# Optimization experiments

Measured on AMD Instinct MI355X. Metric: run time of the kernel, lower is better.

Reference implementation:

```python
import jax, jax.numpy as jnp
import numpy as np

NUM_HEADS = 12   # H
NUM_TASKS = 4    # T
TOP_K = 2        # capacity_factor


def setup_inputs() -> dict:
    key = jax.random.key(0)
    ks = jax.random.split(key, 4)
    B, N, C = 2, 4100, 768  # N = NUM_TASKS + M, M = 4096
    x = jax.random.normal(ks[0], (B, N, C), dtype=jnp.float32)
    # torch.nn.Linear weights are [out_features, in_features]; y = x @ W.T
    qs_w = jax.random.normal(ks[1], (NUM_TASKS, C, C), dtype=jnp.float32) * 0.02
    kv_w = jax.random.normal(ks[2], (2 * C, C), dtype=jnp.float32) * 0.02
    experts_w = jax.random.normal(ks[3], (NUM_TASKS, C, C), dtype=jnp.float32) * 0.02
    return {"x": x, "qs_w": qs_w, "kv_w": kv_w, "experts_w": experts_w}


def reference(x, qs_w, kv_w, experts_w):
    B, N, C = x.shape
    T, H, K = NUM_TASKS, NUM_HEADS, TOP_K
    d = C // H
    M = N - T
    scale = d ** -0.5

    feature = x[:, T:, :]                                    # [B,M,C]
    kv = (feature @ kv_w.T).reshape(B, M, 2, H, d)
    k = jnp.transpose(kv[:, :, 0], (0, 2, 1, 3))             # [B,H,M,d]
    v = jnp.transpose(kv[:, :, 1], (0, 2, 1, 3))             # [B,H,M,d]

    # per-task q projections on task tokens (qs_w[t] is [out,in])
    q = jnp.einsum('btc,toc->bto', x[:, :T], qs_w)           # [B,T,C]
    q = q.reshape(B, T, H, d).transpose(0, 2, 1, 3)          # [B,H,T,d]

    attn = jnp.einsum('bhtd,bhmd->bhtm', q, k) * scale       # [B,H,T,M]
    topv, topi = jax.lax.top_k(attn, K)                      # [B,H,T,K]
    topw = jax.nn.softmax(topv, axis=-1)                     # softmax over top-k only

    # scatter softmaxed top-k back into dense [B,H,T,M] (indices unique per row)
    oh = jax.nn.one_hot(topi, M, dtype=x.dtype)              # [B,H,T,K,M]
    attn_topk = jnp.einsum('bhtk,bhtkm->bhtm', topw, oh)
    attn_token = jnp.einsum('bhtm,bhmd->bhtd', attn_topk, v)
    attn_token = attn_token.transpose(0, 2, 1, 3).reshape(B, T, C)   # [B,T,C]

    # gather top-k feature rows per head/task, weight, and scatter back
    fm = feature.reshape(B, M, H, d).transpose(0, 2, 1, 3)   # [B,H,M,d]
    feat_topk = jnp.take_along_axis(fm[:, :, None], topi[..., None], axis=3)  # [B,H,T,K,d]
    feat_topk = feat_topk * topw[..., None]
    # scatter to [B,H,T,M,d], then permute(0,2,3,1,4)+reshape -> [B,T,M,C]
    feat_pad = jnp.einsum('bhtkd,bhtkm->btmhd', feat_topk, oh).reshape(B, T, M, C)

    # per-task experts (no bias); einsum('btnc,btnc->bnc') with ones = sum over t
    feature_output = jnp.einsum('btmc,toc->bmo', feat_pad, experts_w)  # [B,M,C]
    token_output = jnp.einsum('btc,toc->bto', attn_token, experts_w)   # [B,T,C]

    return jnp.concatenate([token_output, feature_output], axis=1)     # [B,N,C]
```

## Files before the change

### kernel.cpp

```cpp
#include <hip/hip_runtime.h>
#include <math.h>

#define B_ 2
#define N_ 4100
#define C_ 768
#define T_ 4
#define H_ 12
#define D_ 64
#define M_ 4096
#define S_ 48
#define KS_ 6
#define KC_ 128
#define SCALE 0.125f

__device__ __forceinline__ bool better(float va, int ia, float vb, int ib) {
  return (va > vb) || (va == vb && ia < ib);
}

__device__ __forceinline__ void merge2(float& v1, int& i1, float& v2, int& i2,
                                       float ov1, int oi1, float ov2, int oi2) {
  if (better(ov1, oi1, v1, i1)) {
    float tv; int ti;
    tv = v1; ti = i1; v1 = ov1; i1 = oi1; ov1 = tv; oi1 = ti;
    tv = v2; ti = i2; v2 = ov2; i2 = oi2; ov2 = tv; oi2 = ti;
  }
  if (better(ov1, oi1, v2, i2)) { v2 = ov1; i2 = oi1; }
}

__global__ __launch_bounds__(256) void q_kernel(const float* __restrict__ x,
    const float* __restrict__ qs_w, float* __restrict__ qbuf) {
  const int oc = blockIdx.x % 12;
  const int t = (blockIdx.x / 12) % T_;
  const int b = blockIdx.x / (12 * T_);
  const int tid = threadIdx.x;
  __shared__ float xs[C_];
  __shared__ float red[256];
  for (int i = tid; i < C_; i += 256) xs[i] = x[((size_t)b * N_ + t) * C_ + i];
  __syncthreads();
  const int j = tid & 63;
  const int pt = tid >> 6;
  const int o = oc * 64 + j;
  const float* wr = qs_w + ((size_t)t * C_ + o) * C_ + pt * 192;
  float a = 0.f;
  for (int c = 0; c < 192; ++c) a += xs[pt * 192 + c] * wr[c];
  red[tid] = a;
  __syncthreads();
  if (tid < 64) {
    float v = (red[tid] + red[tid + 64] + red[tid + 128] + red[tid + 192]) * SCALE;
    qbuf[((size_t)b * T_ + t) * C_ + o] = v;
  }
}

__global__ __launch_bounds__(256) void qk_kernel(const float* __restrict__ qbuf,
    const float* __restrict__ kv_w, float* __restrict__ qk) {
  const int h = blockIdx.x % H_;
  const int t = (blockIdx.x / H_) % T_;
  const int b = blockIdx.x / (T_ * H_);
  const int tid = threadIdx.x;
  __shared__ float qs[D_];
  if (tid < 64) qs[tid] = qbuf[((size_t)b * T_ + t) * C_ + h * 64 + tid];
  __syncthreads();
  for (int c = tid; c < C_; c += 256) {
    float a = 0.f;
    #pragma unroll 8
    for (int j = 0; j < 64; ++j) a += qs[j] * kv_w[((size_t)(h * 64 + j)) * C_ + c];
    qk[(((size_t)b * T_ + t) * H_ + h) * C_ + c] = a;
  }
}

__global__ __launch_bounds__(256) void score_kernel(const float* __restrict__ x,
    const float* __restrict__ qk, float* __restrict__ part) {
  const int mt = blockIdx.x & 63;
  const int b = blockIdx.x >> 6;
  const int kc = blockIdx.y;
  const int tid = threadIdx.x;
  const int m0 = mt * 64;

  __shared__ __align__(16) float fbuf[64][68];
  __shared__ __align__(16) float qkbuf[48][68];

  const int mg = tid & 15;
  const int sg = tid >> 4;

  float acc[4][3];
  #pragma unroll
  for (int u = 0; u < 4; ++u)
    #pragma unroll
    for (int i = 0; i < 3; ++i) acc[u][i] = 0.f;

  const float* xb = x + ((size_t)b * N_ + T_ + m0) * C_ + kc * KC_;
  const float* qkb = qk + (size_t)b * S_ * C_ + kc * KC_;

  for (int cc = 0; cc < KC_ / 64; ++cc) {
    __syncthreads();
    for (int i = tid; i < 64 * 16; i += 256) {
      int row = i >> 4, c4 = i & 15;
      *(float4*)&fbuf[row][c4 * 4] =
          *(const float4*)(xb + (size_t)row * C_ + cc * 64 + c4 * 4);
    }
    for (int i = tid; i < 48 * 16; i += 256) {
      int s = i >> 4, c4 = i & 15;
      *(float4*)&qkbuf[s][c4 * 4] =
          *(const float4*)(qkb + (size_t)s * C_ + cc * 64 + c4 * 4);
    }
    __syncthreads();
    #pragma unroll 4
    for (int c4 = 0; c4 < 16; ++c4) {
      float4 f[4], q[3];
      f[0] = *(const float4*)&fbuf[mg][c4 * 4];
      f[1] = *(const float4*)&fbuf[mg + 16][c4 * 4];
      f[2] = *(const float4*)&fbuf[mg + 32][c4 * 4];
      f[3] = *(const float4*)&fbuf[mg + 48][c4 * 4];
      q[0] = *(const float4*)&qkbuf[sg * 3 + 0][c4 * 4];
      q[1] = *(const float4*)&qkbuf[sg * 3 + 1][c4 * 4];
      q[2] = *(const float4*)&qkbuf[sg * 3 + 2][c4 * 4];
      #pragma unroll
      for (int u = 0; u < 4; ++u)
        #pragma unroll
        for (int i = 0; i < 3; ++i)
          acc[u][i] += f[u].x * q[i].x + f[u].y * q[i].y +
                       f[u].z * q[i].z + f[u].w * q[i].w;
    }
  }

  #pragma unroll
  for (int i = 0; i < 3; ++i) {
    int s = sg * 3 + i;
    float* pp = part + (((size_t)kc * B_ + b) * S_ + s) * M_ + m0 + mg;
    #pragma unroll
    for (int u = 0; u < 4; ++u) pp[16 * u] = acc[u][i];
  }
}

__global__ __launch_bounds__(256) void top2_kernel(const float* __restrict__ part,
                                                   float* __restrict__ top2) {
  const int s = blockIdx.x % S_;
  const int b = blockIdx.x / S_;
  const int tid = threadIdx.x;
  float v1 = -INFINITY, v2 = -INFINITY;
  int i1 = 0x7fffffff, i2 = 0x7fffffff;
  const float* p0 = part + ((size_t)b * S_ + s) * M_;
  const size_t kstride = (size_t)B_ * S_ * M_;
  for (int m = tid; m < M_; m += 256) {
    float v = 0.f;
    #pragma unroll
    for (int kc = 0; kc < KS_; ++kc) v += p0[kc * kstride + m];
    if (better(v, m, v1, i1)) { v2 = v1; i2 = i1; v1 = v; i1 = m; }
    else if (better(v, m, v2, i2)) { v2 = v; i2 = m; }
  }
  #pragma unroll
  for (int off = 1; off < 64; off <<= 1) {
    float ov1 = __shfl_xor(v1, off);
    int   oi1 = __shfl_xor(i1, off);
    float ov2 = __shfl_xor(v2, off);
    int   oi2 = __shfl_xor(i2, off);
    merge2(v1, i1, v2, i2, ov1, oi1, ov2, oi2);
  }
  __shared__ float cbuf[4][4];
  const int w = tid >> 6, lane = tid & 63;
  if (lane == 0) {
    cbuf[w][0] = v1; ((int*)cbuf[w])[1] = i1;
    cbuf[w][2] = v2; ((int*)cbuf[w])[3] = i2;
  }
  __syncthreads();
  if (tid == 0) {
    for (int ww = 1; ww < 4; ++ww)
      merge2(v1, i1, v2, i2, cbuf[ww][0], ((int*)cbuf[ww])[1],
             cbuf[ww][2], ((int*)cbuf[ww])[3]);
    float w1 = 1.f / (1.f + expf(v2 - v1));
    float* tp = top2 + ((size_t)b * S_ + s) * 4;
    ((int*)tp)[0] = i1; ((int*)tp)[1] = i2;
    tp[2] = w1; tp[3] = 1.f - w1;
  }
}

__global__ __launch_bounds__(256) void gather_kernel(const float* __restrict__ x,
    const float* __restrict__ kv_w, const float* __restrict__ experts_w,
    const float* __restrict__ top2, float* __restrict__ attn, float* __restrict__ out) {
  const int h = blockIdx.x % H_;
  const int t = (blockIdx.x / H_) % T_;
  const int b = blockIdx.x / S_;
  const int tid = threadIdx.x;
  const float* tp = top2 + (size_t)blockIdx.x * 4;
  const int i1 = ((const int*)tp)[0];
  const int i2 = ((const int*)tp)[1];
  const float w1 = tp[2], w2 = tp[3];
  __shared__ float f0[C_], f1[C_], fc[C_], red[256];
  const float* r0 = x + ((size_t)b * N_ + T_ + i1) * C_;
  const float* r1 = x + ((size_t)b * N_ + T_ + i2) * C_;
  for (int i = tid; i < C_; i += 256) {
    float a = r0[i], bb = r1[i];
    f0[i] = a; f1[i] = bb; fc[i] = w1 * a + w2 * bb;
  }
  __syncthreads();
  const int j = tid & 63, pt = tid >> 6;
  {
    const float* kr = kv_w + ((size_t)(C_ + h * 64 + j)) * C_ + pt * 192;
    float a = 0.f;
    for (int c = 0; c < 192; ++c) a += fc[pt * 192 + c] * kr[c];
    red[tid] = a;
  }
  __syncthreads();
  if (tid < 64)
    attn[((size_t)b * T_ + t) * C_ + h * 64 + tid] =
        red[tid] + red[tid + 64] + red[tid + 128] + red[tid + 192];
  const size_t o0 = ((size_t)b * N_ + T_ + i1) * C_;
  const size_t o1 = ((size_t)b * N_ + T_ + i2) * C_;
  for (int o = tid; o < C_; o += 256) {
    const float* er = experts_w + ((size_t)t * C_ + o) * C_ + h * 64;
    float a0 = 0.f, a1 = 0.f;
    #pragma unroll 8
    for (int c = 0; c < 64; ++c) {
      float e = er[c];
      a0 += e * f0[h * 64 + c];
      a1 += e * f1[h * 64 + c];
    }
    atomicAdd(&out[o0 + o], w1 * a0);
    atomicAdd(&out[o1 + o], w2 * a1);
  }
}

__global__ __launch_bounds__(256) void token_kernel(const float* __restrict__ attn,
    const float* __restrict__ experts_w, float* __restrict__ out) {
  const int oc = blockIdx.x % 12;
  const int t = (blockIdx.x / 12) % T_;
  const int b = blockIdx.x / (12 * T_);
  const int tid = threadIdx.x;
  __shared__ float ar[C_];
  __shared__ float red[256];
  for (int i = tid; i < C_; i += 256) ar[i] = attn[((size_t)b * T_ + t) * C_ + i];
  __syncthreads();
  const int j = tid & 63, pt = tid >> 6;
  const int o = oc * 64 + j;
  const float* er = experts_w + ((size_t)t * C_ + o) * C_ + pt * 192;
  float a = 0.f;
  for (int c = 0; c < 192; ++c) a += ar[pt * 192 + c] * er[c];
  red[tid] = a;
  __syncthreads();
  if (tid < 64)
    out[((size_t)b * N_ + t) * C_ + oc * 64 + tid] =
        red[tid] + red[tid + 64] + red[tid + 128] + red[tid + 192];
}

extern "C" void kernel_launch(void* const* d_in, const int* in_sizes, int n_in,
                              void* d_out, int out_size, void* d_ws, size_t ws_size,
                              hipStream_t stream) {
  const float* x         = (const float*)d_in[0];
  const float* qs_w      = (const float*)d_in[1];
  const float* kv_w      = (const float*)d_in[2];
  const float* experts_w = (const float*)d_in[3];
  float* out = (float*)d_out;

  float* ws   = (float*)d_ws;
  float* qbuf = ws;
  float* qk   = qbuf + (size_t)B_ * T_ * C_;
  float* part = qk + (size_t)B_ * S_ * C_;
  float* top2 = part + (size_t)KS_ * B_ * S_ * M_;
  float* attn = top2 + (size_t)B_ * S_ * 4;

  hipMemsetAsync(d_out, 0, (size_t)out_size * sizeof(float), stream);

  hipLaunchKernelGGL(q_kernel,     dim3(B_ * T_ * 12),      dim3(256), 0, stream, x, qs_w, qbuf);
  hipLaunchKernelGGL(qk_kernel,    dim3(B_ * T_ * H_),      dim3(256), 0, stream, qbuf, kv_w, qk);
  hipLaunchKernelGGL(score_kernel, dim3(B_ * 64, KS_),      dim3(256), 0, stream, x, qk, part);
  hipLaunchKernelGGL(top2_kernel,  dim3(B_ * S_),           dim3(256), 0, stream, part, top2);
  hipLaunchKernelGGL(gather_kernel,dim3(B_ * S_),           dim3(256), 0, stream, x, kv_w, experts_w, top2, attn, out);
  hipLaunchKernelGGL(token_kernel, dim3(B_ * T_ * 12),      dim3(256), 0, stream, attn, experts_w, out);
}
```

Measured before the change: 166.4 us.

## Fuse q/qk, top2/gather/token kernels and split score reduction finer

Merges q projection into the qk kernel, with each block recomputing only its head's 64-wide q slice. Folds the top-2 selection and the token expert projection into the gather kernel, which now writes token outputs via atomics. Doubles the score kernel's K-split (KS 12, KC 64) so each block loads one tile, giving more blocks but more partial sums to reduce. Launches drop from six to three, at the cost of more partial-buffer traffic and extra atomics on the token rows.

```diff
diff --git a/kernel.cpp b/kernel.cpp
--- a/kernel.cpp
+++ b/kernel.cpp
@@ -9,8 +9,8 @@
 #define D_ 64
 #define M_ 4096
 #define S_ 48
-#define KS_ 6
-#define KC_ 128
+#define KS_ 12
+#define KC_ 64
 #define SCALE 0.125f
 
 __device__ __forceinline__ bool better(float va, int ia, float vb, int ib) {
@@ -27,44 +27,35 @@
   if (better(ov1, oi1, v2, i2)) { v2 = ov1; i2 = oi1; }
 }
 
-__global__ __launch_bounds__(256) void q_kernel(const float* __restrict__ x,
-    const float* __restrict__ qs_w, float* __restrict__ qbuf) {
-  const int oc = blockIdx.x % 12;
-  const int t = (blockIdx.x / 12) % T_;
-  const int b = blockIdx.x / (12 * T_);
+__global__ __launch_bounds__(256) void qk_kernel(const float* __restrict__ x,
+    const float* __restrict__ qs_w, const float* __restrict__ kv_w,
+    float* __restrict__ qk) {
+  const int h = blockIdx.x % H_;
+  const int t = (blockIdx.x / H_) % T_;
+  const int b = blockIdx.x / S_;
   const int tid = threadIdx.x;
   __shared__ float xs[C_];
   __shared__ float red[256];
+  __shared__ float qseg[D_];
   for (int i = tid; i < C_; i += 256) xs[i] = x[((size_t)b * N_ + t) * C_ + i];
   __syncthreads();
-  const int j = tid & 63;
-  const int pt = tid >> 6;
-  const int o = oc * 64 + j;
-  const float* wr = qs_w + ((size_t)t * C_ + o) * C_ + pt * 192;
-  float a = 0.f;
-  for (int c = 0; c < 192; ++c) a += xs[pt * 192 + c] * wr[c];
-  red[tid] = a;
-  __syncthreads();
-  if (tid < 64) {
-    float v = (red[tid] + red[tid + 64] + red[tid + 128] + red[tid + 192]) * SCALE;
-    qbuf[((size_t)b * T_ + t) * C_ + o] = v;
-  }
-}
-
-__global__ __launch_bounds__(256) void qk_kernel(const float* __restrict__ qbuf,
-    const float* __restrict__ kv_w, float* __restrict__ qk) {
-  const int h = blockIdx.x % H_;
-  const int t = (blockIdx.x / H_) % T_;
-  const int b = blockIdx.x / (T_ * H_);
-  const int tid = threadIdx.x;
-  __shared__ float qs[D_];
-  if (tid < 64) qs[tid] = qbuf[((size_t)b * T_ + t) * C_ + h * 64 + tid];
+  {
+    const int j = tid & 63;
+    const int pt = tid >> 6;
+    const float* wr = qs_w + ((size_t)t * C_ + h * D_ + j) * C_ + pt * 192;
+    float a = 0.f;
+    for (int c = 0; c < 192; ++c) a += xs[pt * 192 + c] * wr[c];
+    red[tid] = a;
+  }
+  __syncthreads();
+  if (tid < 64)
+    qseg[tid] = (red[tid] + red[tid + 64] + red[tid + 128] + red[tid + 192]) * SCALE;
   __syncthreads();
   for (int c = tid; c < C_; c += 256) {
     float a = 0.f;
     #pragma unroll 8
-    for (int j = 0; j < 64; ++j) a += qs[j] * kv_w[((size_t)(h * 64 + j)) * C_ + c];
-    qk[(((size_t)b * T_ + t) * H_ + h) * C_ + c] = a;
+    for (int j = 0; j < 64; ++j) a += qseg[j] * kv_w[((size_t)(h * D_ + j)) * C_ + c];
+    qk[((size_t)blockIdx.x) * C_ + c] = a;
   }
 }
 
@@ -79,6 +70,21 @@
   __shared__ __align__(16) float fbuf[64][68];
   __shared__ __align__(16) float qkbuf[48][68];
 
+  const float* xb = x + ((size_t)b * N_ + T_ + m0) * C_ + kc * KC_;
+  const float* qkb = qk + (size_t)b * S_ * C_ + kc * KC_;
+
+  for (int i = tid; i < 64 * 16; i += 256) {
+    int row = i >> 4, c4 = i & 15;
+    *(float4*)&fbuf[row][c4 * 4] =
+        *(const float4*)(xb + (size_t)row * C_ + c4 * 4);
+  }
+  for (int i = tid; i < 48 * 16; i += 256) {
+    int s = i >> 4, c4 = i & 15;
+    *(float4*)&qkbuf[s][c4 * 4] =
+        *(const float4*)(qkb + (size_t)s * C_ + c4 * 4);
+  }
+  __syncthreads();
+
   const int mg = tid & 15;
   const int sg = tid >> 4;
 
@@ -88,39 +94,22 @@
     #pragma unroll
     for (int i = 0; i < 3; ++i) acc[u][i] = 0.f;
 
-  const float* xb = x + ((size_t)b * N_ + T_ + m0) * C_ + kc * KC_;
-  const float* qkb = qk + (size_t)b * S_ * C_ + kc * KC_;
-
-  for (int cc = 0; cc < KC_ / 64; ++cc) {
-    __syncthreads();
-    for (int i = tid; i < 64 * 16; i += 256) {
-      int row = i >> 4, c4 = i & 15;
-      *(float4*)&fbuf[row][c4 * 4] =
-          *(const float4*)(xb + (size_t)row * C_ + cc * 64 + c4 * 4);
-    }
-    for (int i = tid; i < 48 * 16; i += 256) {
-      int s = i >> 4, c4 = i & 15;
-      *(float4*)&qkbuf[s][c4 * 4] =
-          *(const float4*)(qkb + (size_t)s * C_ + cc * 64 + c4 * 4);
-    }
-    __syncthreads();
-    #pragma unroll 4
-    for (int c4 = 0; c4 < 16; ++c4) {
-      float4 f[4], q[3];
-      f[0] = *(const float4*)&fbuf[mg][c4 * 4];
-      f[1] = *(const float4*)&fbuf[mg + 16][c4 * 4];
-      f[2] = *(const float4*)&fbuf[mg + 32][c4 * 4];
-      f[3] = *(const float4*)&fbuf[mg + 48][c4 * 4];
-      q[0] = *(const float4*)&qkbuf[sg * 3 + 0][c4 * 4];
-      q[1] = *(const float4*)&qkbuf[sg * 3 + 1][c4 * 4];
-      q[2] = *(const float4*)&qkbuf[sg * 3 + 2][c4 * 4];
+  #pragma unroll 4
+  for (int c4 = 0; c4 < 16; ++c4) {
+    float4 f[4], q[3];
+    f[0] = *(const float4*)&fbuf[mg][c4 * 4];
+    f[1] = *(const float4*)&fbuf[mg + 16][c4 * 4];
+    f[2] = *(const float4*)&fbuf[mg + 32][c4 * 4];
+    f[3] = *(const float4*)&fbuf[mg + 48][c4 * 4];
+    q[0] = *(const float4*)&qkbuf[sg * 3 + 0][c4 * 4];
+    q[1] = *(const float4*)&qkbuf[sg * 3 + 1][c4 * 4];
+    q[2] = *(const float4*)&qkbuf[sg * 3 + 2][c4 * 4];
+    #pragma unroll
+    for (int u = 0; u < 4; ++u)
       #pragma unroll
-      for (int u = 0; u < 4; ++u)
-        #pragma unroll
-        for (int i = 0; i < 3; ++i)
-          acc[u][i] += f[u].x * q[i].x + f[u].y * q[i].y +
-                       f[u].z * q[i].z + f[u].w * q[i].w;
-    }
+      for (int i = 0; i < 3; ++i)
+        acc[u][i] += f[u].x * q[i].x + f[u].y * q[i].y +
+                     f[u].z * q[i].z + f[u].w * q[i].w;
   }
 
   #pragma unroll
@@ -132,60 +121,59 @@
   }
 }
 
-__global__ __launch_bounds__(256) void top2_kernel(const float* __restrict__ part,
-                                                   float* __restrict__ top2) {
-  const int s = blockIdx.x % S_;
-  const int b = blockIdx.x / S_;
-  const int tid = threadIdx.x;
-  float v1 = -INFINITY, v2 = -INFINITY;
-  int i1 = 0x7fffffff, i2 = 0x7fffffff;
-  const float* p0 = part + ((size_t)b * S_ + s) * M_;
-  const size_t kstride = (size_t)B_ * S_ * M_;
-  for (int m = tid; m < M_; m += 256) {
-    float v = 0.f;
-    #pragma unroll
-    for (int kc = 0; kc < KS_; ++kc) v += p0[kc * kstride + m];
-    if (better(v, m, v1, i1)) { v2 = v1; i2 = i1; v1 = v; i1 = m; }
-    else if (better(v, m, v2, i2)) { v2 = v; i2 = m; }
-  }
-  #pragma unroll
-  for (int off = 1; off < 64; off <<= 1) {
-    float ov1 = __shfl_xor(v1, off);
-    int   oi1 = __shfl_xor(i1, off);
-    float ov2 = __shfl_xor(v2, off);
-    int   oi2 = __shfl_xor(i2, off);
-    merge2(v1, i1, v2, i2, ov1, oi1, ov2, oi2);
-  }
-  __shared__ float cbuf[4][4];
-  const int w = tid >> 6, lane = tid & 63;
-  if (lane == 0) {
-    cbuf[w][0] = v1; ((int*)cbuf[w])[1] = i1;
-    cbuf[w][2] = v2; ((int*)cbuf[w])[3] = i2;
-  }
-  __syncthreads();
-  if (tid == 0) {
-    for (int ww = 1; ww < 4; ++ww)
-      merge2(v1, i1, v2, i2, cbuf[ww][0], ((int*)cbuf[ww])[1],
-             cbuf[ww][2], ((int*)cbuf[ww])[3]);
-    float w1 = 1.f / (1.f + expf(v2 - v1));
-    float* tp = top2 + ((size_t)b * S_ + s) * 4;
-    ((int*)tp)[0] = i1; ((int*)tp)[1] = i2;
-    tp[2] = w1; tp[3] = 1.f - w1;
-  }
-}
-
 __global__ __launch_bounds__(256) void gather_kernel(const float* __restrict__ x,
     const float* __restrict__ kv_w, const float* __restrict__ experts_w,
-    const float* __restrict__ top2, float* __restrict__ attn, float* __restrict__ out) {
+    const float* __restrict__ part, float* __restrict__ out) {
   const int h = blockIdx.x % H_;
   const int t = (blockIdx.x / H_) % T_;
   const int b = blockIdx.x / S_;
   const int tid = threadIdx.x;
-  const float* tp = top2 + (size_t)blockIdx.x * 4;
-  const int i1 = ((const int*)tp)[0];
-  const int i2 = ((const int*)tp)[1];
-  const float w1 = tp[2], w2 = tp[3];
+
   __shared__ float f0[C_], f1[C_], fc[C_], red[256];
+  __shared__ float attnh[D_];
+  __shared__ float cbuf[4][4];
+  __shared__ float sel[4];
+
+  {
+    float v1 = -INFINITY, v2 = -INFINITY;
+    int i1 = 0x7fffffff, i2 = 0x7fffffff;
+    const float* p0 = part + ((size_t)b * S_ + (t * H_ + h)) * M_;
+    const size_t kstride = (size_t)B_ * S_ * M_;
+    for (int m = tid; m < M_; m += 256) {
+      float v = 0.f;
+      #pragma unroll
+      for (int kc = 0; kc < KS_; ++kc) v += p0[kc * kstride + m];
+      if (better(v, m, v1, i1)) { v2 = v1; i2 = i1; v1 = v; i1 = m; }
+      else if (better(v, m, v2, i2)) { v2 = v; i2 = m; }
+    }
+    #pragma unroll
+    for (int off = 1; off < 64; off <<= 1) {
+      float ov1 = __shfl_xor(v1, off);
+      int   oi1 = __shfl_xor(i1, off);
+      float ov2 = __shfl_xor(v2, off);
+      int   oi2 = __shfl_xor(i2, off);
+      merge2(v1, i1, v2, i2, ov1, oi1, ov2, oi2);
+    }
+    const int w = tid >> 6, lane = tid & 63;
+    if (lane == 0) {
+      cbuf[w][0] = v1; ((int*)cbuf[w])[1] = i1;
+      cbuf[w][2] = v2; ((int*)cbuf[w])[3] = i2;
+    }
+    __syncthreads();
+    if (tid == 0) {
+      for (int ww = 1; ww < 4; ++ww)
+        merge2(v1, i1, v2, i2, cbuf[ww][0], ((int*)cbuf[ww])[1],
+               cbuf[ww][2], ((int*)cbuf[ww])[3]);
+      float w1 = 1.f / (1.f + expf(v2 - v1));
+      ((int*)sel)[0] = i1; ((int*)sel)[1] = i2;
+      sel[2] = w1; sel[3] = 1.f - w1;
+    }
+    __syncthreads();
+  }
+  const int i1 = ((const int*)sel)[0];
+  const int i2 = ((const int*)sel)[1];
+  const float w1 = sel[2], w2 = sel[3];
+
   const float* r0 = x + ((size_t)b * N_ + T_ + i1) * C_;
   const float* r1 = x + ((size_t)b * N_ + T_ + i2) * C_;
   for (int i = tid; i < C_; i += 256) {
@@ -193,53 +181,36 @@
     f0[i] = a; f1[i] = bb; fc[i] = w1 * a + w2 * bb;
   }
   __syncthreads();
+
   const int j = tid & 63, pt = tid >> 6;
   {
-    const float* kr = kv_w + ((size_t)(C_ + h * 64 + j)) * C_ + pt * 192;
+    const float* kr = kv_w + ((size_t)(C_ + h * D_ + j)) * C_ + pt * 192;
     float a = 0.f;
     for (int c = 0; c < 192; ++c) a += fc[pt * 192 + c] * kr[c];
     red[tid] = a;
   }
   __syncthreads();
   if (tid < 64)
-    attn[((size_t)b * T_ + t) * C_ + h * 64 + tid] =
-        red[tid] + red[tid + 64] + red[tid + 128] + red[tid + 192];
+    attnh[tid] = red[tid] + red[tid + 64] + red[tid + 128] + red[tid + 192];
+  __syncthreads();
+
+  const size_t ot = ((size_t)b * N_ + t) * C_;
   const size_t o0 = ((size_t)b * N_ + T_ + i1) * C_;
   const size_t o1 = ((size_t)b * N_ + T_ + i2) * C_;
   for (int o = tid; o < C_; o += 256) {
-    const float* er = experts_w + ((size_t)t * C_ + o) * C_ + h * 64;
-    float a0 = 0.f, a1 = 0.f;
+    const float* er = experts_w + ((size_t)t * C_ + o) * C_ + h * D_;
+    float at = 0.f, a0 = 0.f, a1 = 0.f;
     #pragma unroll 8
-    for (int c = 0; c < 64; ++c) {
+    for (int c = 0; c < D_; ++c) {
       float e = er[c];
-      a0 += e * f0[h * 64 + c];
-      a1 += e * f1[h * 64 + c];
-    }
+      at += e * attnh[c];
+      a0 += e * f0[h * D_ + c];
+      a1 += e * f1[h * D_ + c];
+    }
+    atomicAdd(&out[ot + o], at);
     atomicAdd(&out[o0 + o], w1 * a0);
     atomicAdd(&out[o1 + o], w2 * a1);
   }
-}
-
-__global__ __launch_bounds__(256) void token_kernel(const float* __restrict__ attn,
-    const float* __restrict__ experts_w, float* __restrict__ out) {
-  const int oc = blockIdx.x % 12;
-  const int t = (blockIdx.x / 12) % T_;
-  const int b = blockIdx.x / (12 * T_);
-  const int tid = threadIdx.x;
-  __shared__ float ar[C_];
-  __shared__ float red[256];
-  for (int i = tid; i < C_; i += 256) ar[i] = attn[((size_t)b * T_ + t) * C_ + i];
-  __syncthreads();
-  const int j = tid & 63, pt = tid >> 6;
-  const int o = oc * 64 + j;
-  const float* er = experts_w + ((size_t)t * C_ + o) * C_ + pt * 192;
-  float a = 0.f;
-  for (int c = 0; c < 192; ++c) a += ar[pt * 192 + c] * er[c];
-  red[tid] = a;
-  __syncthreads();
-  if (tid < 64)
-    out[((size_t)b * N_ + t) * C_ + oc * 64 + tid] =
-        red[tid] + red[tid + 64] + red[tid + 128] + red[tid + 192];
 }
 
 extern "C" void kernel_launch(void* const* d_in, const int* in_sizes, int n_in,
@@ -252,18 +223,12 @@
   float* out = (float*)d_out;
 
   float* ws   = (float*)d_ws;
-  float* qbuf = ws;
-  float* qk   = qbuf + (size_t)B_ * T_ * C_;
+  float* qk   = ws;
   float* part = qk + (size_t)B_ * S_ * C_;
-  float* top2 = part + (size_t)KS_ * B_ * S_ * M_;
-  float* attn = top2 + (size_t)B_ * S_ * 4;
 
   hipMemsetAsync(d_out, 0, (size_t)out_size * sizeof(float), stream);
 
-  hipLaunchKernelGGL(q_kernel,     dim3(B_ * T_ * 12),      dim3(256), 0, stream, x, qs_w, qbuf);
-  hipLaunchKernelGGL(qk_kernel,    dim3(B_ * T_ * H_),      dim3(256), 0, stream, qbuf, kv_w, qk);
-  hipLaunchKernelGGL(score_kernel, dim3(B_ * 64, KS_),      dim3(256), 0, stream, x, qk, part);
-  hipLaunchKernelGGL(top2_kernel,  dim3(B_ * S_),           dim3(256), 0, stream, part, top2);
-  hipLaunchKernelGGL(gather_kernel,dim3(B_ * S_),           dim3(256), 0, stream, x, kv_w, experts_w, top2, attn, out);
-  hipLaunchKernelGGL(token_kernel, dim3(B_ * T_ * 12),      dim3(256), 0, stream, attn, experts_w, out);
-}
+  hipLaunchKernelGGL(qk_kernel,    dim3(B_ * S_),      dim3(256), 0, stream, x, qs_w, kv_w, qk);
+  hipLaunchKernelGGL(score_kernel, dim3(B_ * 64, KS_), dim3(256), 0, stream, x, qk, part);
+  hipLaunchKernelGGL(gather_kernel,dim3(B_ * S_),      dim3(256), 0, stream, x, kv_w, experts_w, part, out);
+}
```

Result: faster. 153.3 us (-7.9%).
